# Optimization experiments

Measured on AMD Instinct MI355X. Metric: run time of the kernel, lower is better.

Reference implementation:

```python
import jax, jax.numpy as jnp
import numpy as np

EPS_KERNEL = 1e-4
EPS_DENOM = 1e-8


def setup_inputs() -> dict:
    key = jax.random.key(0)
    k1, k2, k3, k4 = jax.random.split(key, 4)
    b, h, n, d = 4, 8, 8192, 64
    nb_features = 266
    return {
        "q": jax.random.normal(k1, (b, h, n, d), dtype=jnp.float32),
        "k": jax.random.normal(k2, (b, h, n, d), dtype=jnp.float32),
        "v": jax.random.normal(k3, (b, h, n, d), dtype=jnp.float32),
        "proj": jax.random.normal(k4, (nb_features, d), dtype=jnp.float32),
    }


def _softmax_kernel(data, proj, is_query):
    # data: [b,h,n,d], proj: [f,d]
    d = data.shape[-1]
    data_normalizer = d ** (-0.25)
    ratio = proj.shape[0] ** (-0.5)
    data_dash = jnp.einsum('bhid,jd->bhij', data_normalizer * data, proj)  # [b,h,n,f]
    diag_data = (jnp.sum(data * data, axis=-1) * 0.5 * data_normalizer ** 2)[..., None]
    if is_query:
        return ratio * (jnp.exp(data_dash - diag_data
                                - jnp.max(data_dash, axis=-1, keepdims=True)) + EPS_KERNEL)
    return ratio * jnp.exp(data_dash - diag_data + EPS_KERNEL)


def reference(q, k, v, proj):
    qp = _softmax_kernel(q, proj, is_query=True)   # [b,h,n,f]
    kp = _softmax_kernel(k, proj, is_query=False)  # [b,h,n,f]
    # non-causal linear attention (never materializes the n x n matrix)
    context = jnp.einsum('bhnf,bhne->bhfe', kp, v)              # [b,h,f,e]
    d_inv = 1.0 / (jnp.einsum('bhnf,bhf->bhn', qp, kp.sum(axis=-2)) + EPS_DENOM)
    return jnp.einsum('bhfe,bhnf,bhn->bhne', context, qp, d_inv)  # [b,h,n,e]
```

## Files before the change

### kernel.cpp

```cpp
#include <hip/hip_runtime.h>
#include <hip/hip_bf16.h>
#include <math.h>


typedef __attribute__((ext_vector_type(8))) short s16x8;
typedef __attribute__((ext_vector_type(4))) float f32x4;

#define MFMA16(a,b,c) __builtin_amdgcn_mfma_f32_16x16x32_bf16((a),(b),(c),0,0,0)

__device__ __forceinline__ unsigned short bf16rne(float x){
  union { __hip_bfloat16 b; unsigned short u; } cv;
  cv.b = __float2bfloat16(x);
  return cv.u;
}
__device__ __forceinline__ float bf16tof(unsigned short h){
  return __uint_as_float(((unsigned)h) << 16);
}
__device__ __forceinline__ float exp2_fast(float x){
#if __has_builtin(__builtin_amdgcn_exp2f)
  return __builtin_amdgcn_exp2f(x);
#else
  float r; asm("v_exp_f32 %0, %1" : "=v"(r) : "v"(x)); return r;
#endif
}
__device__ __forceinline__ float rcp_fast(float x){
#if __has_builtin(__builtin_amdgcn_rcpf)
  return __builtin_amdgcn_rcpf(x);
#else
  return 1.0f / x;
#endif
}
__device__ __forceinline__ void cvt_hl8(const float v[8], s16x8& h, s16x8& l){
  #pragma unroll
  for(int j=0;j<8;++j){
    unsigned short hh = bf16rne(v[j]);
    h[j] = (short)hh;
    l[j] = (short)bf16rne(v[j] - bf16tof(hh));
  }
}
__device__ __forceinline__ void cvt_h8(const float v[8], s16x8& h){
  #pragma unroll
  for(int j=0;j<8;++j) h[j] = (short)bf16rne(v[j]);
}

__global__ void fa21_prep(const float* __restrict__ proj, short* __restrict__ ph,
                          float pscale){
  int idx = blockIdx.x*256 + threadIdx.x;
  if(idx >= 288*64) return;
  int f = idx >> 6, dc = idx & 63;
  float v = (f < 266) ? proj[f*64 + dc]*pscale : 0.f;
  ph[idx] = (short)bf16rne(v);
}

__global__ __launch_bounds__(1024,1) void fa21_p1(
    const float* __restrict__ kin, const float* __restrict__ vin,
    const short* __restrict__ pjh,
    float* __restrict__ ctx_part, float* __restrict__ ksum_part,
    float koff, float diagc){
  extern __shared__ char smem[];
  char* sph = smem;
  char* skh = smem + 40960;
  float* ex = (float*)smem;
  const int tid = threadIdx.x;
  const int w = tid >> 6, lane = tid & 63, g = lane >> 4, q = lane & 15;
  const int bid = blockIdx.x;
  const int head = bid & 31, chunk = bid >> 5;
  for(int i = tid; i < 2560; i += 1024){
    int f = i >> 3;
    int byt = (f*128 + (i & 7)*16) ^ ((f & 7) << 4);
    s16x8 vh8 = {0,0,0,0,0,0,0,0};
    if(f < 288) vh8 = ((const s16x8*)pjh)[i];
    *(s16x8*)(sph + byt) = vh8;
  }
  const int mtp = w & 3, fqp = w >> 2;
  const int et  = w & 3, fqc = w >> 2;
  f32x4 acc[5];
  #pragma unroll
  for(int a=0;a<5;++a){ f32x4 z = {0.f,0.f,0.f,0.f}; acc[a] = z; }
  float ksacc[5] = {0.f,0.f,0.f,0.f,0.f};
  const float* kbase = kin + (size_t)head*8192*64;
  const float* vbase = vin + (size_t)head*8192*64;
  const float* xp  = kbase + (size_t)(chunk*1024 + mtp*16 + q)*64 + g*8;
  const float* vp  = vbase + (size_t)(chunk*1024 + 8*g)*64 + et*16 + q;
  const float* vp2 = vp + 2048;
  float4 xa0 = *(const float4*)(xp);
  float4 xb0 = *(const float4*)(xp + 4);
  float4 xa1 = *(const float4*)(xp + 32);
  float4 xb1 = *(const float4*)(xp + 36);
  __syncthreads();
  #pragma unroll 1
  for(int it = 0; it < 16; ++it){
    char* kcur = skh + (it & 1)*40960;
    s16x8 xh[2], xl[2];
    float diag;
    {
      float v0[8] = {xa0.x,xa0.y,xa0.z,xa0.w,xb0.x,xb0.y,xb0.z,xb0.w};
      float v1[8] = {xa1.x,xa1.y,xa1.z,xa1.w,xb1.x,xb1.y,xb1.z,xb1.w};
      float ss = 0.f;
      #pragma unroll
      for(int j=0;j<8;++j){ ss += v0[j]*v0[j]; ss += v1[j]*v1[j]; }
      cvt_hl8(v0, xh[0], xl[0]);
      cvt_hl8(v1, xh[1], xl[1]);
      ss += __shfl_xor(ss, 16); ss += __shfl_xor(ss, 32);
      diag = ss * diagc;
    }
    float dro[4];
    #pragma unroll
    for(int i=0;i<4;++i) dro[i] = __shfl(diag, 4*g + i) - koff;
    s16x8 vh[2];
    {
      float vv[8];
      #pragma unroll
      for(int i2=0;i2<8;++i2) vv[i2] = vp[i2*64];
      cvt_h8(vv, vh[0]);
      #pragma unroll
      for(int i2=0;i2<8;++i2) vv[i2] = vp2[i2*64];
      cvt_h8(vv, vh[1]);
    }
    vp += 4096; vp2 += 4096;
    f32x4 S[5];
    #pragma unroll
    for(int t=0;t<5;++t){ f32x4 z = {0.f,0.f,0.f,0.f}; S[t] = z; }
    #pragma unroll
    for(int t=0; t<5; ++t){
      const int gt = fqp*5 + t;
      if(gt > 16) continue;
      const int f = gt*16 + q;
      #pragma unroll
      for(int ks=0; ks<2; ++ks){
        int byt = (f*128 + ks*64 + g*16) ^ ((f & 7) << 4);
        s16x8 bph = *(const s16x8*)(sph + byt);
        S[t] = MFMA16(xh[ks], bph, S[t]);
        S[t] = MFMA16(xl[ks], bph, S[t]);
      }
    }
    #pragma unroll
    for(int t=0; t<5; ++t){
      const int gt = fqp*5 + t;
      if(gt > 16) continue;
      const int f = gt*16 + q;
      float p[4];
      #pragma unroll
      for(int i=0;i<4;++i) p[i] = exp2_fast(S[t][i] - dro[i]);
      if(gt == 16){
        #pragma unroll
        for(int i=0;i<4;++i) p[i] = (q < 10) ? p[i] : 0.f;
      }
      ksacc[t] += p[0]+p[1]+p[2]+p[3];
      uint2 hv;
      hv.x = (unsigned)bf16rne(p[0]) | ((unsigned)bf16rne(p[1]) << 16);
      hv.y = (unsigned)bf16rne(p[2]) | ((unsigned)bf16rne(p[3]) << 16);
      int byt = (f*128 + (mtp*16 + 4*g)*2) ^ ((f & 7) << 4);
      *(uint2*)(kcur + byt) = hv;
    }
    xp += 4096;
    if(it < 15){
      xa0 = *(const float4*)(xp);
      xb0 = *(const float4*)(xp + 4);
      xa1 = *(const float4*)(xp + 32);
      xb1 = *(const float4*)(xp + 36);
    }
    __syncthreads();
    #pragma unroll
    for(int fm=0; fm<5; ++fm){
      const int gt = fqc*5 + fm;
      if(gt > 16) continue;
      const int fg = gt*16 + q;
      #pragma unroll
      for(int ks=0; ks<2; ++ks){
        int byt = (fg*128 + ks*64 + g*16) ^ ((fg & 7) << 4);
        s16x8 kf = *(const s16x8*)(kcur + byt);
        acc[fm] = MFMA16(kf, vh[ks], acc[fm]);
      }
    }
  }
  {
    float* cp = ctx_part + (size_t)bid*288*64;
    #pragma unroll
    for(int fm=0; fm<5; ++fm){
      const int gt = fqc*5 + fm;
      if(gt < 18){
        #pragma unroll
        for(int i=0;i<4;++i){
          int f = gt*16 + 4*g + i;
          cp[f*64 + et*16 + q] = acc[fm][i];
        }
      }
    }
  }
  __syncthreads();
  #pragma unroll
  for(int t=0; t<5; ++t){
    float s = ksacc[t];
    s += __shfl_xor(s, 16); s += __shfl_xor(s, 32);
    if(g == 0) ex[mtp*320 + (fqp*5 + t)*16 + q] = s;
  }
  __syncthreads();
  for(int i = tid; i < 288; i += 1024)
    ksum_part[(size_t)bid*288 + i] = ex[i] + ex[320+i] + ex[640+i] + ex[960+i];
}

__global__ void fa21_reduce(const float* __restrict__ ctx_part, const float* __restrict__ ksum_part,
                            short* __restrict__ cth, float* __restrict__ ksum){
  int h = blockIdx.x >> 3, sl = blockIdx.x & 7, tid = threadIdx.x;
  for(int j = tid; j < 288*8; j += 256){
    int idx = sl*288*8 + j;
    float s = 0.f;
    #pragma unroll
    for(int c=0;c<8;++c) s += ctx_part[(size_t)(h + 32*c)*288*64 + idx];
    int f = idx >> 6, e = idx & 63;
    cth[(size_t)h*64*288 + e*288 + f] = (short)bf16rne(s);
  }
  if(sl == 0){
    for(int idx = tid; idx < 288; idx += 256){
      float s = 0.f;
      #pragma unroll
      for(int c=0;c<8;++c) s += ksum_part[(size_t)(h + 32*c)*288 + idx];
      ksum[h*288 + idx] = s;
    }
  }
}

__global__ __launch_bounds__(1024,1) void fa21_p2(
    const float* __restrict__ qin,
    const short* __restrict__ pjh,
    const short* __restrict__ cth,
    const float* __restrict__ ksum, float* __restrict__ outp,
    float qoff, float qeps, float diagc){
  extern __shared__ char smem[];
  char* sct = smem;
  char* sqp = smem + 44032;
  float* rmx = (float*)(smem + 88064);
  float* dnb = (float*)(smem + 89088);
  float* sks = (float*)(smem + 90112);
  const int tid = threadIdx.x;
  const int w = tid >> 6, lane = tid & 63, g = lane >> 4, q = lane & 15;
  const int bid = blockIdx.x;
  const int head = bid & 31, chunk = bid >> 5;
  const int mt4 = w & 3, fq = w >> 2;
  {
    const short* cb = cth + (size_t)head*18432;
    for(int i = tid; i < 2560; i += 1024){
      int e = i / 40, j = i - e*40;
      int f0 = j*8;
      s16x8 v8 = {0,0,0,0,0,0,0,0};
      if(f0 < 288) v8 = *(const s16x8*)(cb + e*288 + f0);
      *(s16x8*)(sct + e*688 + f0*2) = v8;
    }
  }
  for(int i = tid; i < 64*8; i += 1024){
    int r = i >> 3, dwi = i & 7;
    *(unsigned*)(sqp + r*688 + 544 + dwi*4) = 0u;
  }
  for(int i = tid; i < 320; i += 1024) sks[i] = (i < 288) ? ksum[head*288 + i] : 0.f;
  s16x8 aph[5][2];
  #pragma unroll
  for(int t=0; t<5; ++t){
    const int f = (fq*5 + t)*16 + q;
    #pragma unroll
    for(int ks=0; ks<2; ++ks){
      s16x8 v8 = {0,0,0,0,0,0,0,0};
      if(f < 288) v8 = *(const s16x8*)(pjh + f*64 + ks*32 + g*8);
      aph[t][ks] = v8;
    }
  }
  const float* qbase = qin + (size_t)head*8192*64;
  float* obase = outp + (size_t)head*8192*64;
  const float* xp = qbase + (size_t)(chunk*1024 + mt4*16 + q)*64 + g*8;
  float* op = obase + (size_t)(chunk*1024 + mt4*16 + 4*g)*64 + fq*16 + q;
  const int nrow = mt4*16 + q;
  float4 xa0 = *(const float4*)(xp);
  float4 xb0 = *(const float4*)(xp + 4);
  float4 xa1 = *(const float4*)(xp + 32);
  float4 xb1 = *(const float4*)(xp + 36);
  xp += 4096;
  __syncthreads();
  #pragma unroll 1
  for(int it=0; it<16; ++it){
    s16x8 xh[2], xl[2];
    float diag;
    {
      float v0[8] = {xa0.x,xa0.y,xa0.z,xa0.w,xb0.x,xb0.y,xb0.z,xb0.w};
      float v1[8] = {xa1.x,xa1.y,xa1.z,xa1.w,xb1.x,xb1.y,xb1.z,xb1.w};
      float ss = 0.f;
      #pragma unroll
      for(int j=0;j<8;++j){ ss += v0[j]*v0[j]; ss += v1[j]*v1[j]; }
      cvt_hl8(v0, xh[0], xl[0]);
      cvt_hl8(v1, xh[1], xl[1]);
      ss += __shfl_xor(ss, 16); ss += __shfl_xor(ss, 32);
      diag = ss * diagc;
    }
    if(it < 15){
      xa0 = *(const float4*)(xp);
      xb0 = *(const float4*)(xp + 4);
      xa1 = *(const float4*)(xp + 32);
      xb1 = *(const float4*)(xp + 36);
      xp += 4096;
    }
    f32x4 S[5];
    #pragma unroll
    for(int t=0;t<5;++t){ f32x4 z = {0.f,0.f,0.f,0.f}; S[t] = z; }
    #pragma unroll
    for(int t=0; t<5; ++t){
      if(fq*5 + t > 16) continue;
      #pragma unroll
      for(int ks=0; ks<2; ++ks){
        S[t] = MFMA16(aph[t][ks], xh[ks], S[t]);
        S[t] = MFMA16(aph[t][ks], xl[ks], S[t]);
      }
    }
    float m = -3e38f;
    #pragma unroll
    for(int t=0; t<5; ++t){
      const int gt = fq*5 + t;
      if(gt > 16) continue;
      if(gt == 16){
        const int fb = gt*16 + 4*g;
        #pragma unroll
        for(int i=0;i<4;++i){
          float v = (fb + i < 266) ? S[t][i] : -3e38f;
          m = fmaxf(m, v);
        }
      } else {
        m = fmaxf(m, fmaxf(fmaxf(S[t][0], S[t][1]), fmaxf(S[t][2], S[t][3])));
      }
    }
    m = fmaxf(m, __shfl_xor(m, 16));
    m = fmaxf(m, __shfl_xor(m, 32));
    if(lane < 16) rmx[fq*64 + nrow] = m;
    __syncthreads();
    float rm = fmaxf(fmaxf(rmx[nrow], rmx[64 + nrow]),
                     fmaxf(rmx[128 + nrow], rmx[192 + nrow]));
    const float dro = diag + rm - qoff;
    float dnp = 0.f;
    #pragma unroll
    for(int t=0; t<5; ++t){
      const int gt = fq*5 + t;
      if(gt > 16) continue;
      const int fb = gt*16 + 4*g;
      f32x4 kv = *(const f32x4*)(sks + fb);
      float pe[4];
      #pragma unroll
      for(int i=0;i<4;++i){
        pe[i] = exp2_fast(S[t][i] - dro) + qeps;
        dnp += pe[i] * kv[i];
      }
      uint2 hv;
      hv.x = (unsigned)bf16rne(pe[0]) | ((unsigned)bf16rne(pe[1]) << 16);
      hv.y = (unsigned)bf16rne(pe[2]) | ((unsigned)bf16rne(pe[3]) << 16);
      *(uint2*)(sqp + nrow*688 + fb*2) = hv;
    }
    dnp += __shfl_xor(dnp, 16);
    dnp += __shfl_xor(dnp, 32);
    if(lane < 16) dnb[fq*64 + nrow] = dnp;
    __syncthreads();
    f32x4 dsum;
    {
      f32x4 d0 = *(const f32x4*)(dnb +       mt4*16 + 4*g);
      f32x4 d1 = *(const f32x4*)(dnb +  64 + mt4*16 + 4*g);
      f32x4 d2 = *(const f32x4*)(dnb + 128 + mt4*16 + 4*g);
      f32x4 d3 = *(const f32x4*)(dnb + 192 + mt4*16 + 4*g);
      #pragma unroll
      for(int i=0;i<4;++i) dsum[i] = d0[i] + d1[i] + d2[i] + d3[i];
    }
    f32x4 oacc = {0.f,0.f,0.f,0.f};
    #pragma unroll
    for(int ks=0; ks<9; ++ks){
      s16x8 ah = *(const s16x8*)(sqp + (mt4*16 + q)*688 + ks*64 + g*16);
      s16x8 ch = *(const s16x8*)(sct + (fq*16 + q)*688 + ks*64 + g*16);
      oacc = MFMA16(ah, ch, oacc);
    }
    #pragma unroll
    for(int i=0;i<4;++i){
      op[i*64] = oacc[i] * rcp_fast(dsum[i] + 1e-8f);
    }
    op += 4096;
  }
}

extern "C" void kernel_launch(void* const* d_in, const int* in_sizes, int n_in,
                              void* d_out, int out_size, void* d_ws, size_t ws_size,
                              hipStream_t stream){
  const float* q    = (const float*)d_in[0];
  const float* k    = (const float*)d_in[1];
  const float* v    = (const float*)d_in[2];
  const float* proj = (const float*)d_in[3];
  float* out = (float*)d_out;
  char* ws = (char*)d_ws;
  short* wproj_h = (short*)(ws);
  float* wctx    = (float*)(ws + 73728);
  float* wksump  = (float*)(ws + 18948096);
  short* wct_h   = (short*)(ws + 19243008);
  float* wksum   = (float*)(ws + 20422656);

  const double LOG2E = 1.4426950408889634;
  const double ln_ratio = -0.5*log(266.0);
  float pscale = (float)(pow(64.0, -0.25) * LOG2E);
  float diagc  = (float)(0.0625 * LOG2E);
  float koff   = (float)((1e-4 + ln_ratio) * LOG2E);
  float qoff   = (float)(ln_ratio * LOG2E);
  float qeps   = (float)(1e-4 / sqrt(266.0));

  hipFuncSetAttribute((const void*)fa21_p1, hipFuncAttributeMaxDynamicSharedMemorySize, 122880);
  hipFuncSetAttribute((const void*)fa21_p2, hipFuncAttributeMaxDynamicSharedMemorySize, 91392);

  fa21_prep<<<72, 256, 0, stream>>>(proj, wproj_h, pscale);
  fa21_p1<<<256, 1024, 122880, stream>>>(k, v, wproj_h, wctx, wksump, koff, diagc);
  fa21_reduce<<<256, 256, 0, stream>>>(wctx, wksump, wct_h, wksum);
  fa21_p2<<<256, 1024, 91392, stream>>>(q, wproj_h, wct_h, wksum, out,
                                        qoff, qeps, diagc);
}
```

Baseline: 165.9 us.

## Process two 64-row query tiles per iteration in phase-2 kernel

Measured after the change: 193.9 us. +16.9%, slower.

```diff
diff --git a/kernel.cpp b/kernel.cpp
--- a/kernel.cpp
+++ b/kernel.cpp
@@ -230,9 +230,9 @@
   extern __shared__ char smem[];
   char* sct = smem;
   char* sqp = smem + 44032;
-  float* rmx = (float*)(smem + 88064);
-  float* dnb = (float*)(smem + 89088);
-  float* sks = (float*)(smem + 90112);
+  float* rmx = (float*)(smem + 119808);
+  float* dnb = (float*)(smem + 121856);
+  float* sks = (float*)(smem + 123904);
   const int tid = threadIdx.x;
   const int w = tid >> 6, lane = tid & 63, g = lane >> 4, q = lane & 15;
   const int bid = blockIdx.x;
@@ -248,9 +248,9 @@
       *(s16x8*)(sct + e*688 + f0*2) = v8;
     }
   }
-  for(int i = tid; i < 64*8; i += 1024){
+  for(int i = tid; i < 128*8; i += 1024){
     int r = i >> 3, dwi = i & 7;
-    *(unsigned*)(sqp + r*688 + 544 + dwi*4) = 0u;
+    *(unsigned*)(sqp + r*592 + 544 + dwi*4) = 0u;
   }
   for(int i = tid; i < 320; i += 1024) sks[i] = (i < 288) ? ksum[head*288 + i] : 0.f;
   s16x8 aph[5][2];
@@ -266,115 +266,206 @@
   }
   const float* qbase = qin + (size_t)head*8192*64;
   float* obase = outp + (size_t)head*8192*64;
-  const float* xp = qbase + (size_t)(chunk*1024 + mt4*16 + q)*64 + g*8;
-  float* op = obase + (size_t)(chunk*1024 + mt4*16 + 4*g)*64 + fq*16 + q;
-  const int nrow = mt4*16 + q;
-  float4 xa0 = *(const float4*)(xp);
-  float4 xb0 = *(const float4*)(xp + 4);
-  float4 xa1 = *(const float4*)(xp + 32);
-  float4 xb1 = *(const float4*)(xp + 36);
-  xp += 4096;
+  const float* xpA = qbase + (size_t)(chunk*1024 + mt4*32 + q)*64 + g*8;
+  const float* xpB = xpA + 1024;
+  float* op = obase + (size_t)(chunk*1024 + mt4*32 + 4*g)*64 + fq*16 + q;
+  const int nrowA = mt4*32 + q;
+  const int nrowB = nrowA + 16;
+  float4 ra = *(const float4*)(xpA);
+  float4 rb = *(const float4*)(xpA + 4);
+  float4 rc = *(const float4*)(xpA + 32);
+  float4 rd = *(const float4*)(xpA + 36);
   __syncthreads();
   #pragma unroll 1
-  for(int it=0; it<16; ++it){
-    s16x8 xh[2], xl[2];
-    float diag;
-    {
-      float v0[8] = {xa0.x,xa0.y,xa0.z,xa0.w,xb0.x,xb0.y,xb0.z,xb0.w};
-      float v1[8] = {xa1.x,xa1.y,xa1.z,xa1.w,xb1.x,xb1.y,xb1.z,xb1.w};
-      float ss = 0.f;
-      #pragma unroll
-      for(int j=0;j<8;++j){ ss += v0[j]*v0[j]; ss += v1[j]*v1[j]; }
-      cvt_hl8(v0, xh[0], xl[0]);
-      cvt_hl8(v1, xh[1], xl[1]);
-      ss += __shfl_xor(ss, 16); ss += __shfl_xor(ss, 32);
-      diag = ss * diagc;
-    }
-    if(it < 15){
-      xa0 = *(const float4*)(xp);
-      xb0 = *(const float4*)(xp + 4);
-      xa1 = *(const float4*)(xp + 32);
-      xb1 = *(const float4*)(xp + 36);
-      xp += 4096;
-    }
-    f32x4 S[5];
-    #pragma unroll
-    for(int t=0;t<5;++t){ f32x4 z = {0.f,0.f,0.f,0.f}; S[t] = z; }
-    #pragma unroll
-    for(int t=0; t<5; ++t){
-      if(fq*5 + t > 16) continue;
-      #pragma unroll
-      for(int ks=0; ks<2; ++ks){
-        S[t] = MFMA16(aph[t][ks], xh[ks], S[t]);
-        S[t] = MFMA16(aph[t][ks], xl[ks], S[t]);
-      }
-    }
-    float m = -3e38f;
-    #pragma unroll
-    for(int t=0; t<5; ++t){
-      const int gt = fq*5 + t;
-      if(gt > 16) continue;
-      if(gt == 16){
+  for(int it=0; it<8; ++it){
+    f32x4 SA[5], SB[5];
+    float diagA, diagB;
+    float mA = -3e38f, mB = -3e38f;
+    {
+      s16x8 xh[2], xl[2];
+      {
+        float v0[8] = {ra.x,ra.y,ra.z,ra.w,rb.x,rb.y,rb.z,rb.w};
+        float v1[8] = {rc.x,rc.y,rc.z,rc.w,rd.x,rd.y,rd.z,rd.w};
+        float ss = 0.f;
+        #pragma unroll
+        for(int j=0;j<8;++j){ ss += v0[j]*v0[j]; ss += v1[j]*v1[j]; }
+        cvt_hl8(v0, xh[0], xl[0]);
+        cvt_hl8(v1, xh[1], xl[1]);
+        ss += __shfl_xor(ss, 16); ss += __shfl_xor(ss, 32);
+        diagA = ss * diagc;
+      }
+      ra = *(const float4*)(xpB);
+      rb = *(const float4*)(xpB + 4);
+      rc = *(const float4*)(xpB + 32);
+      rd = *(const float4*)(xpB + 36);
+      xpB += 8192;
+      #pragma unroll
+      for(int t=0;t<5;++t){ f32x4 z = {0.f,0.f,0.f,0.f}; SA[t] = z; }
+      #pragma unroll
+      for(int t=0; t<5; ++t){
+        if(fq*5 + t > 16) continue;
+        #pragma unroll
+        for(int ks=0; ks<2; ++ks){
+          SA[t] = MFMA16(aph[t][ks], xh[ks], SA[t]);
+          SA[t] = MFMA16(aph[t][ks], xl[ks], SA[t]);
+        }
+      }
+      #pragma unroll
+      for(int t=0; t<5; ++t){
+        const int gt = fq*5 + t;
+        if(gt > 16) continue;
+        if(gt == 16){
+          const int fb = gt*16 + 4*g;
+          #pragma unroll
+          for(int i=0;i<4;++i){
+            float v = (fb + i < 266) ? SA[t][i] : -3e38f;
+            mA = fmaxf(mA, v);
+          }
+        } else {
+          mA = fmaxf(mA, fmaxf(fmaxf(SA[t][0], SA[t][1]), fmaxf(SA[t][2], SA[t][3])));
+        }
+      }
+      mA = fmaxf(mA, __shfl_xor(mA, 16));
+      mA = fmaxf(mA, __shfl_xor(mA, 32));
+      if(lane < 16) rmx[fq*128 + nrowA] = mA;
+    }
+    {
+      s16x8 xh[2], xl[2];
+      {
+        float v0[8] = {ra.x,ra.y,ra.z,ra.w,rb.x,rb.y,rb.z,rb.w};
+        float v1[8] = {rc.x,rc.y,rc.z,rc.w,rd.x,rd.y,rd.z,rd.w};
+        float ss = 0.f;
+        #pragma unroll
+        for(int j=0;j<8;++j){ ss += v0[j]*v0[j]; ss += v1[j]*v1[j]; }
+        cvt_hl8(v0, xh[0], xl[0]);
+        cvt_hl8(v1, xh[1], xl[1]);
+        ss += __shfl_xor(ss, 16); ss += __shfl_xor(ss, 32);
+        diagB = ss * diagc;
+      }
+      xpA += 8192;
+      if(it < 7){
+        ra = *(const float4*)(xpA);
+        rb = *(const float4*)(xpA + 4);
+        rc = *(const float4*)(xpA + 32);
+        rd = *(const float4*)(xpA + 36);
+      }
+      #pragma unroll
+      for(int t=0;t<5;++t){ f32x4 z = {0.f,0.f,0.f,0.f}; SB[t] = z; }
+      #pragma unroll
+      for(int t=0; t<5; ++t){
+        if(fq*5 + t > 16) continue;
+        #pragma unroll
+        for(int ks=0; ks<2; ++ks){
+          SB[t] = MFMA16(aph[t][ks], xh[ks], SB[t]);
+          SB[t] = MFMA16(aph[t][ks], xl[ks], SB[t]);
+        }
+      }
+      #pragma unroll
+      for(int t=0; t<5; ++t){
+        const int gt = fq*5 + t;
+        if(gt > 16) continue;
+        if(gt == 16){
+          const int fb = gt*16 + 4*g;
+          #pragma unroll
+          for(int i=0;i<4;++i){
+            float v = (fb + i < 266) ? SB[t][i] : -3e38f;
+            mB = fmaxf(mB, v);
+          }
+        } else {
+          mB = fmaxf(mB, fmaxf(fmaxf(SB[t][0], SB[t][1]), fmaxf(SB[t][2], SB[t][3])));
+        }
+      }
+      mB = fmaxf(mB, __shfl_xor(mB, 16));
+      mB = fmaxf(mB, __shfl_xor(mB, 32));
+      if(lane < 16) rmx[fq*128 + nrowB] = mB;
+    }
+    __syncthreads();
+    {
+      float rm = fmaxf(fmaxf(rmx[nrowA], rmx[128 + nrowA]),
+                       fmaxf(rmx[256 + nrowA], rmx[384 + nrowA]));
+      const float dro = diagA + rm - qoff;
+      float dnp = 0.f;
+      #pragma unroll
+      for(int t=0; t<5; ++t){
+        const int gt = fq*5 + t;
+        if(gt > 16) continue;
         const int fb = gt*16 + 4*g;
+        f32x4 kv = *(const f32x4*)(sks + fb);
+        float pe[4];
         #pragma unroll
         for(int i=0;i<4;++i){
-          float v = (fb + i < 266) ? S[t][i] : -3e38f;
-          m = fmaxf(m, v);
-        }
-      } else {
-        m = fmaxf(m, fmaxf(fmaxf(S[t][0], S[t][1]), fmaxf(S[t][2], S[t][3])));
-      }
-    }
-    m = fmaxf(m, __shfl_xor(m, 16));
-    m = fmaxf(m, __shfl_xor(m, 32));
-    if(lane < 16) rmx[fq*64 + nrow] = m;
+          pe[i] = exp2_fast(SA[t][i] - dro) + qeps;
+          dnp += pe[i] * kv[i];
+        }
+        uint2 hv;
+        hv.x = (unsigned)bf16rne(pe[0]) | ((unsigned)bf16rne(pe[1]) << 16);
+        hv.y = (unsigned)bf16rne(pe[2]) | ((unsigned)bf16rne(pe[3]) << 16);
+        *(uint2*)(sqp + nrowA*592 + fb*2) = hv;
+      }
+      dnp += __shfl_xor(dnp, 16);
+      dnp += __shfl_xor(dnp, 32);
+      if(lane < 16) dnb[fq*128 + nrowA] = dnp;
+    }
+    {
+      float rm = fmaxf(fmaxf(rmx[nrowB], rmx[128 + nrowB]),
+                       fmaxf(rmx[256 + nrowB], rmx[384 + nrowB]));
+      const float dro = diagB + rm - qoff;
+      float dnp = 0.f;
+      #pragma unroll
+      for(int t=0; t<5; ++t){
+        const int gt = fq*5 + t;
+        if(gt > 16) continue;
+        const int fb = gt*16 + 4*g;
+        f32x4 kv = *(const f32x4*)(sks + fb);
+        float pe[4];
+        #pragma unroll
+        for(int i=0;i<4;++i){
+          pe[i] = exp2_fast(SB[t][i] - dro) + qeps;
+          dnp += pe[i] * kv[i];
+        }
+        uint2 hv;
+        hv.x = (unsigned)bf16rne(pe[0]) | ((unsigned)bf16rne(pe[1]) << 16);
+        hv.y = (unsigned)bf16rne(pe[2]) | ((unsigned)bf16rne(pe[3]) << 16);
+        *(uint2*)(sqp + nrowB*592 + fb*2) = hv;
+      }
+      dnp += __shfl_xor(dnp, 16);
+      dnp += __shfl_xor(dnp, 32);
+      if(lane < 16) dnb[fq*128 + nrowB] = dnp;
+    }
     __syncthreads();
-    float rm = fmaxf(fmaxf(rmx[nrow], rmx[64 + nrow]),
-                     fmaxf(rmx[128 + nrow], rmx[192 + nrow]));
-    const float dro = diag + rm - qoff;
-    float dnp = 0.f;
-    #pragma unroll
-    for(int t=0; t<5; ++t){
-      const int gt = fq*5 + t;
-      if(gt > 16) continue;
-      const int fb = gt*16 + 4*g;
-      f32x4 kv = *(const f32x4*)(sks + fb);
-      float pe[4];
+    f32x4 dsumA, dsumB;
+    {
+      const int rb4 = mt4*32 + 4*g;
+      f32x4 a0 = *(const f32x4*)(dnb +       rb4);
+      f32x4 a1 = *(const f32x4*)(dnb + 128 + rb4);
+      f32x4 a2 = *(const f32x4*)(dnb + 256 + rb4);
+      f32x4 a3 = *(const f32x4*)(dnb + 384 + rb4);
+      f32x4 b0 = *(const f32x4*)(dnb +       rb4 + 16);
+      f32x4 b1 = *(const f32x4*)(dnb + 128 + rb4 + 16);
+      f32x4 b2 = *(const f32x4*)(dnb + 256 + rb4 + 16);
+      f32x4 b3 = *(const f32x4*)(dnb + 384 + rb4 + 16);
       #pragma unroll
       for(int i=0;i<4;++i){
-        pe[i] = exp2_fast(S[t][i] - dro) + qeps;
-        dnp += pe[i] * kv[i];
-      }
-      uint2 hv;
-      hv.x = (unsigned)bf16rne(pe[0]) | ((unsigned)bf16rne(pe[1]) << 16);
-      hv.y = (unsigned)bf16rne(pe[2]) | ((unsigned)bf16rne(pe[3]) << 16);
-      *(uint2*)(sqp + nrow*688 + fb*2) = hv;
-    }
-    dnp += __shfl_xor(dnp, 16);
-    dnp += __shfl_xor(dnp, 32);
-    if(lane < 16) dnb[fq*64 + nrow] = dnp;
-    __syncthreads();
-    f32x4 dsum;
-    {
-      f32x4 d0 = *(const f32x4*)(dnb +       mt4*16 + 4*g);
-      f32x4 d1 = *(const f32x4*)(dnb +  64 + mt4*16 + 4*g);
-      f32x4 d2 = *(const f32x4*)(dnb + 128 + mt4*16 + 4*g);
-      f32x4 d3 = *(const f32x4*)(dnb + 192 + mt4*16 + 4*g);
-      #pragma unroll
-      for(int i=0;i<4;++i) dsum[i] = d0[i] + d1[i] + d2[i] + d3[i];
-    }
-    f32x4 oacc = {0.f,0.f,0.f,0.f};
+        dsumA[i] = a0[i] + a1[i] + a2[i] + a3[i];
+        dsumB[i] = b0[i] + b1[i] + b2[i] + b3[i];
+      }
+    }
+    f32x4 oaccA = {0.f,0.f,0.f,0.f};
+    f32x4 oaccB = {0.f,0.f,0.f,0.f};
     #pragma unroll
     for(int ks=0; ks<9; ++ks){
-      s16x8 ah = *(const s16x8*)(sqp + (mt4*16 + q)*688 + ks*64 + g*16);
       s16x8 ch = *(const s16x8*)(sct + (fq*16 + q)*688 + ks*64 + g*16);
-      oacc = MFMA16(ah, ch, oacc);
+      s16x8 aA = *(const s16x8*)(sqp + (mt4*32 + q)*592 + ks*64 + g*16);
+      s16x8 aB = *(const s16x8*)(sqp + (mt4*32 + 16 + q)*592 + ks*64 + g*16);
+      oaccA = MFMA16(aA, ch, oaccA);
+      oaccB = MFMA16(aB, ch, oaccB);
     }
     #pragma unroll
     for(int i=0;i<4;++i){
-      op[i*64] = oacc[i] * rcp_fast(dsum[i] + 1e-8f);
-    }
-    op += 4096;
+      op[i*64]        = oaccA[i] * rcp_fast(dsumA[i] + 1e-8f);
+      op[i*64 + 1024] = oaccB[i] * rcp_fast(dsumB[i] + 1e-8f);
+    }
+    op += 8192;
   }
 }
 
@@ -402,11 +493,11 @@
   float qeps   = (float)(1e-4 / sqrt(266.0));
 
   hipFuncSetAttribute((const void*)fa21_p1, hipFuncAttributeMaxDynamicSharedMemorySize, 122880);
-  hipFuncSetAttribute((const void*)fa21_p2, hipFuncAttributeMaxDynamicSharedMemorySize, 91392);
+  hipFuncSetAttribute((const void*)fa21_p2, hipFuncAttributeMaxDynamicSharedMemorySize, 125184);
 
   fa21_prep<<<72, 256, 0, stream>>>(proj, wproj_h, pscale);
   fa21_p1<<<256, 1024, 122880, stream>>>(k, v, wproj_h, wctx, wksump, koff, diagc);
   fa21_reduce<<<256, 256, 0, stream>>>(wctx, wksump, wct_h, wksum);
-  fa21_p2<<<256, 1024, 91392, stream>>>(q, wproj_h, wct_h, wksum, out,
-                                        qoff, qeps, diagc);
-}
+  fa21_p2<<<256, 1024, 125184, stream>>>(q, wproj_h, wct_h, wksum, out,
+                                         qoff, qeps, diagc);
+}
```
